# Kernel optimization log

Hardware: AMD Instinct MI355X
Metric: run time of the kernel (lower is better)

Reference implementation:

```python
import jax, jax.numpy as jnp
import numpy as np

B, S, H, T, W = 8, 512, 768, 4, 10
NEG = -1e9

def _u(key, shape, k):
    return jax.random.uniform(key, shape, jnp.float32, -k, k)

def setup_inputs():
    key = jax.random.key(0)
    ks = jax.random.split(key, 20)
    kh = float(1.0 / np.sqrt(H)); kt = float(1.0 / np.sqrt(T))
    return dict(
        embeddings=jax.random.normal(ks[0], (B, S, H), jnp.float32),
        l1f_wih=_u(ks[1], (4 * H, H), kh), l1f_whh=_u(ks[2], (4 * H, H), kh), l1f_b=_u(ks[3], (4 * H,), kh),
        l1r_wih=_u(ks[4], (4 * H, H), kh), l1r_whh=_u(ks[5], (4 * H, H), kh), l1r_b=_u(ks[6], (4 * H,), kh),
        attn_w=_u(ks[7], (3 * H,), kh), attn_b=_u(ks[8], (1,), kh),
        l2f_wih=_u(ks[9], (4 * T, 2 * H), kt), l2f_whh=_u(ks[10], (4 * T, T), kt), l2f_b=_u(ks[11], (4 * T,), kt),
        l2r_wih=_u(ks[12], (4 * T, 2 * H), kt), l2r_whh=_u(ks[13], (4 * T, T), kt), l2r_b=_u(ks[14], (4 * T,), kt),
        crf_start=0.1 * jax.random.normal(ks[15], (T,), jnp.float32),
        crf_end=0.1 * jax.random.normal(ks[16], (T,), jnp.float32),
        crf_trans=0.1 * jax.random.normal(ks[17], (T, T), jnp.float32),
        window_size=W,
    )

def _lstm_dir(x, w_ih, w_hh, b):
    # x: [B,S,D] -> [B,S,Hh]; torch gate order i,f,g,o
    Hh = w_hh.shape[1]
    bs = x.shape[0]
    xs = (jnp.einsum('bsd,gd->bsg', x, w_ih) + b).transpose(1, 0, 2)  # [S,B,4Hh]
    def step(carry, xt):
        h, c = carry
        g = xt + h @ w_hh.T
        i, f, gg, o = jnp.split(g, 4, axis=-1)
        c = jax.nn.sigmoid(f) * c + jax.nn.sigmoid(i) * jnp.tanh(gg)
        h = jax.nn.sigmoid(o) * jnp.tanh(c)
        return (h, c), h
    init = (jnp.zeros((bs, Hh), x.dtype), jnp.zeros((bs, Hh), x.dtype))
    _, hs = jax.lax.scan(step, init, xs)
    return hs.transpose(1, 0, 2)

def _bilstm(x, pf, pr):
    hf = _lstm_dir(x, *pf)
    hr = _lstm_dir(x[:, ::-1], *pr)[:, ::-1]
    return jnp.concatenate([hf, hr], axis=-1)

def _win_attn(h, w, b, win):
    # h: [B,S,D]; similarity(hi,hj) = w1.hi + w2.hj + w3.(hi*hj) + b
    bs, s, d = h.shape
    w1, w2, w3 = w[:d], w[d:2 * d], w[2 * d:]
    offs = jnp.arange(-win, win + 1)                      # [K]
    idx = jnp.arange(s)[:, None] + offs[None, :]          # [S,K]
    valid = (idx >= 0) & (idx < s)
    idxc = jnp.clip(idx, 0, s - 1)
    hw = h[:, idxc]                                       # [B,S,K,D]
    scores = (h @ w1)[:, :, None] \
        + jnp.einsum('bskd,d->bsk', hw, w2) \
        + jnp.einsum('bsd,bskd->bsk', h * w3, hw) + b[0]
    scores = jnp.where(valid[None], scores, NEG)
    aw = jax.nn.softmax(scores, axis=-1)                  # [B,S,K]
    return jnp.einsum('bsk,bskd->bsd', aw, hw)

def _viterbi(em, start, end, trans):
    # em: [B,S,T] -> tags [B,S]
    score0 = start[None] + em[:, 0]
    ems = em.transpose(1, 0, 2)[1:]                       # [S-1,B,T]
    def step(score, e_t):
        nxt = score[:, :, None] + trans[None]             # [B,Tprev,T]
        best = jnp.max(nxt, axis=1) + e_t
        bp = jnp.argmax(nxt, axis=1)
        return best, bp
    final, bps = jax.lax.scan(step, score0, ems)          # bps [S-1,B,T]
    final = final + end[None]
    last = jnp.argmax(final, axis=-1)                     # [B]
    def back(tag, bp):
        prev = jnp.take_along_axis(bp, tag[:, None], axis=1)[:, 0]
        return prev, prev
    _, tags_rev = jax.lax.scan(back, last, bps[::-1])
    return jnp.concatenate([tags_rev[::-1], last[None]], axis=0).transpose(1, 0)

def reference(embeddings, l1f_wih, l1f_whh, l1f_b, l1r_wih, l1r_whh, l1r_b,
              attn_w, attn_b, l2f_wih, l2f_whh, l2f_b, l2r_wih, l2r_whh, l2r_b,
              crf_start, crf_end, crf_trans, window_size):
    h1 = _bilstm(embeddings, (l1f_wih, l1f_whh, l1f_b), (l1r_wih, l1r_whh, l1r_b))
    d = h1.shape[-1] // 2
    hs = h1[..., :d] + h1[..., d:]                        # sum of directions [B,S,H]
    att = _win_attn(hs, attn_w, attn_b, int(window_size))
    x2 = jnp.concatenate([hs, att], axis=-1)              # [B,S,2H]
    h2 = _bilstm(x2, (l2f_wih, l2f_whh, l2f_b), (l2r_wih, l2r_whh, l2r_b))
    d2 = h2.shape[-1] // 2
    em = h2[..., :d2] + h2[..., d2:]                      # CRF emissions [B,S,T]
    tags = _viterbi(em, crf_start, crf_end, crf_trans)
    return tags, em
```

## Files before the change

### kernel.cpp

```cpp
#include <hip/hip_runtime.h>
#include <math.h>

#define SEQ 512
#define BATCH 8
#define HID 768
#define G4 3072
#define CHUNK 128
#define NEGV (-1000000000.0f)

typedef float v4f __attribute__((ext_vector_type(4)));

__device__ __forceinline__ float sigm(float x) { return 1.0f / (1.0f + expf(-x)); }

__device__ __forceinline__ float wred(float x) {
#pragma unroll
  for (int off = 32; off > 0; off >>= 1) x += __shfl_xor(x, off, 64);
  return x;
}

__device__ __forceinline__ void load2_f4_sc(const float* p0, const float* p1,
                                            v4f& a, v4f& b) {
  asm volatile("global_load_dwordx4 %0, %2, off sc0 sc1\n\t"
               "global_load_dwordx4 %1, %3, off sc0 sc1\n\t"
               "s_waitcnt vmcnt(0)"
               : "=&v"(a), "=&v"(b) : "v"(p0), "v"(p1) : "memory");
}
__device__ __forceinline__ int load_i_sc(const int* p) {
  int r;
  asm volatile("global_load_dword %0, %1, off sc0 sc1\n\ts_waitcnt vmcnt(0)"
               : "=v"(r) : "v"(p) : "memory");
  return r;
}
__device__ __forceinline__ void store_f_sc(float* p, float v) {
  asm volatile("global_store_dword %0, %1, off sc0 sc1" :: "v"(p), "v"(v) : "memory");
}
__device__ __forceinline__ void store_i_sc(int* p, int v) {
  asm volatile("global_store_dword %0, %1, off sc0 sc1" :: "v"(p), "v"(v) : "memory");
}

template <int CTRL, int RMASK>
__device__ __forceinline__ float dpp_add(float x) {
  int y = __builtin_amdgcn_update_dpp(0, __float_as_int(x), CTRL, RMASK, 0xF, false);
  return x + __int_as_float(y);
}
__device__ __forceinline__ float reduce32(float x) {
  x = dpp_add<0x121, 0xF>(x);
  x = dpp_add<0x122, 0xF>(x);
  x = dpp_add<0x124, 0xF>(x);
  x = dpp_add<0x128, 0xF>(x);
  x = dpp_add<0x142, 0xA>(x);
  return x;
}

__global__ void k_init(float* __restrict__ hbuf, int* __restrict__ flags) {
  int i = blockIdx.x * blockDim.x + threadIdx.x;
  if (i < 2 * 2 * BATCH * HID) hbuf[i] = 0.0f;
  if (i < 4096) flags[i] = 0;
}

__global__ __launch_bounds__(256) void k_proj1(
    const float* __restrict__ emb,
    const float* __restrict__ w_f, const float* __restrict__ b_f,
    const float* __restrict__ w_r, const float* __restrict__ b_r,
    float* __restrict__ xs_f, float* __restrict__ xs_r, int chunk) {
  __shared__ float As[16][132];
  __shared__ float Bs[16][132];
  const int tid = threadIdx.x;
  const int bn0 = blockIdx.x * 128;
  const int bb  = blockIdx.y;
  const int dir = blockIdx.z;
  const float* W    = dir ? w_r : w_f;
  const float* bias = dir ? b_r : b_f;
  float* xs = dir ? xs_r : xs_f;

  float acc[8][8];
#pragma unroll
  for (int i = 0; i < 8; i++)
#pragma unroll
    for (int j = 0; j < 8; j++) acc[i][j] = 0.0f;

  const int mload = tid & 127;
  const int kq0   = tid >> 7;
  const int tglob = dir ? (SEQ - 1 - (chunk * CHUNK + mload)) : (chunk * CHUNK + mload);
  const float* arow = emb + (size_t)(bb * SEQ + tglob) * HID;
  const float* brow = W + (size_t)(bn0 + mload) * HID;
  const int tm = tid & 15, tn = tid >> 4;

  for (int kt = 0; kt < HID; kt += 16) {
#pragma unroll
    for (int rep = 0; rep < 2; rep++) {
      int kq = kq0 + rep * 2;
      float4 a = *(const float4*)(arow + kt + kq * 4);
      As[kq * 4 + 0][mload] = a.x; As[kq * 4 + 1][mload] = a.y;
      As[kq * 4 + 2][mload] = a.z; As[kq * 4 + 3][mload] = a.w;
      float4 b = *(const float4*)(brow + kt + kq * 4);
      Bs[kq * 4 + 0][mload] = b.x; Bs[kq * 4 + 1][mload] = b.y;
      Bs[kq * 4 + 2][mload] = b.z; Bs[kq * 4 + 3][mload] = b.w;
    }
    __syncthreads();
#pragma unroll
    for (int k = 0; k < 16; k++) {
      float4 a0 = *(const float4*)&As[k][tm * 8];
      float4 a1 = *(const float4*)&As[k][tm * 8 + 4];
      float4 b0 = *(const float4*)&Bs[k][tn * 8];
      float4 b1 = *(const float4*)&Bs[k][tn * 8 + 4];
      float av[8] = {a0.x, a0.y, a0.z, a0.w, a1.x, a1.y, a1.z, a1.w};
      float bv[8] = {b0.x, b0.y, b0.z, b0.w, b1.x, b1.y, b1.z, b1.w};
#pragma unroll
      for (int i = 0; i < 8; i++)
#pragma unroll
        for (int j = 0; j < 8; j++) acc[i][j] += av[i] * bv[j];
    }
    __syncthreads();
  }
#pragma unroll
  for (int i = 0; i < 8; i++) {
    int row = tm * 8 + i;
    size_t base = (size_t)(bb * CHUNK + row) * G4 + bn0 + tn * 8;
#pragma unroll
    for (int j = 0; j < 8; j++) xs[base + j] = acc[i][j] + bias[bn0 + tn * 8 + j];
  }
}

__global__ __launch_bounds__(384, 2) void k_rec1(
    const float* __restrict__ whh_f, const float* __restrict__ whh_r,
    const float* __restrict__ xs_f, const float* __restrict__ xs_r,
    float* __restrict__ hbuf, float* __restrict__ cbuf, int* __restrict__ flags,
    float* __restrict__ hf, float* __restrict__ hr, int t0, int init) {
  __shared__ float hlds[4 * HID];
  __shared__ float psl[192];
  const int tid = threadIdx.x;
  const int bid = blockIdx.x;
  const int dir = bid >> 7;
  const int bh  = (bid >> 6) & 1;
  const int jb  = bid & 63;
  const int J0  = jb * 12;
  const int grp = dir * 2 + bh;
  const int g  = tid >> 5;
  const int kq = tid & 31;
  const int j  = J0 + g;
  const int ej = tid >> 2;
  const int eb = tid & 3;

  const float* W  = dir ? whh_r : whh_f;
  const float* xs = dir ? xs_r  : xs_f;
  float* harr = dir ? hr : hf;

  float wreg[4][24];
#pragma unroll
  for (int gate = 0; gate < 4; gate++) {
#pragma unroll
    for (int q = 0; q < 6; q++) {
      *(v4f*)&wreg[gate][q * 4] =
          *(const v4f*)&W[(size_t)(gate * HID + j) * HID + q * 128 + kq * 4];
    }
  }

  float cc = 0.0f;
  if (!init && tid < 48) cc = cbuf[bid * 48 + tid];

  for (int stp = 0; stp < CHUNK; stp++) {
    const int s = t0 + stp;
    const int par = s & 1;

    float exs0 = 0.f, exs1 = 0.f, exs2 = 0.f, exs3 = 0.f;
    if (tid < 48) {
      const size_t xbase = (size_t)((bh * 4 + eb) * CHUNK + stp) * G4 + J0 + ej;
      exs0 = xs[xbase + 0 * HID];
      exs1 = xs[xbase + 1 * HID];
      exs2 = xs[xbase + 2 * HID];
      exs3 = xs[xbase + 3 * HID];
    }
    if (tid < 64) {
      const int* fp = flags + (grp * 64 + tid) * 16;
      while (load_i_sc(fp) < s) { __builtin_amdgcn_s_sleep(1); }
    }
    __syncthreads();

    {
      const float* src = hbuf + (size_t)((par * 2 + dir) * BATCH + bh * 4) * HID + tid * 8;
      v4f a, b4;
      load2_f4_sc(src, src + 4, a, b4);
      *(v4f*)&hlds[tid * 8]     = a;
      *(v4f*)&hlds[tid * 8 + 4] = b4;
    }
    __syncthreads();

    float hk[4][24];
#pragma unroll
    for (int b = 0; b < 4; b++)
#pragma unroll
      for (int q = 0; q < 6; q++)
        *(v4f*)&hk[b][q * 4] = *(const v4f*)&hlds[b * HID + q * 128 + kq * 4];

    float acc[4][4];
#pragma unroll
    for (int gate = 0; gate < 4; gate++)
#pragma unroll
      for (int b = 0; b < 4; b++) acc[gate][b] = 0.0f;
#pragma unroll
    for (int b = 0; b < 4; b++)
#pragma unroll
      for (int gate = 0; gate < 4; gate++)
#pragma unroll
        for (int k = 0; k < 24; k++) acc[gate][b] += wreg[gate][k] * hk[b][k];

#pragma unroll
    for (int gate = 0; gate < 4; gate++)
#pragma unroll
      for (int b = 0; b < 4; b++) acc[gate][b] = reduce32(acc[gate][b]);

    if (kq == 16) {
#pragma unroll
      for (int gate = 0; gate < 4; gate++)
#pragma unroll
        for (int b = 0; b < 4; b++) psl[(g * 4 + gate) * 4 + b] = acc[gate][b];
    }
    __syncthreads();

    if (tid < 48) {
      float iv = psl[(ej * 4 + 0) * 4 + eb] + exs0;
      float fv = psl[(ej * 4 + 1) * 4 + eb] + exs1;
      float gv = psl[(ej * 4 + 2) * 4 + eb] + exs2;
      float ov = psl[(ej * 4 + 3) * 4 + eb] + exs3;
      cc = sigm(fv) * cc + sigm(iv) * tanhf(gv);
      float h = sigm(ov) * tanhf(cc);
      const int t = dir ? (SEQ - 1 - s) : s;
      const int bg = bh * 4 + eb;
      store_f_sc(hbuf + (size_t)(((par ^ 1) * 2 + dir) * BATCH + bg) * HID + J0 + ej, h);
      harr[(size_t)(bg * SEQ + t) * HID + J0 + ej] = h;
    }
    if (tid < 64) {
      asm volatile("s_waitcnt vmcnt(0)" ::: "memory");
      if (tid == 0) store_i_sc(flags + (grp * 64 + jb) * 16, s + 1);
    }
  }
  if (tid < 48) cbuf[bid * 48 + tid] = cc;
}

__global__ __launch_bounds__(64) void k_attn(
    const float* __restrict__ hf, const float* __restrict__ hr,
    const float* __restrict__ attn_w, const float* __restrict__ attn_b,
    float* __restrict__ att) {
  const int l = threadIdx.x;
  const int s = blockIdx.x, b = blockIdx.y;
  const size_t rbase = (size_t)(b * SEQ + s) * HID;
  float v[12];
  float u1p = 0.0f;
#pragma unroll
  for (int jj = 0; jj < 12; jj++) {
    int d = l + 64 * jj;
    float x = hf[rbase + d] + hr[rbase + d];
    u1p += x * attn_w[d];
    v[jj] = attn_w[HID + d] + x * attn_w[2 * HID + d];
  }
  float u1 = wred(u1p) + attn_b[0];
  float sc[21];
  for (int o = 0; o < 21; o++) {
    int s2 = s + o - 10;
    if (s2 >= 0 && s2 < SEQ) {
      const size_t b2 = (size_t)(b * SEQ + s2) * HID;
      float p = 0.0f;
#pragma unroll
      for (int jj = 0; jj < 12; jj++) {
        int d = l + 64 * jj;
        p += (hf[b2 + d] + hr[b2 + d]) * v[jj];
      }
      sc[o] = wred(p) + u1;
    } else {
      sc[o] = NEGV;
    }
  }
  float m = sc[0];
#pragma unroll
  for (int o = 1; o < 21; o++) m = fmaxf(m, sc[o]);
  float sum = 0.0f;
#pragma unroll
  for (int o = 0; o < 21; o++) { sc[o] = expf(sc[o] - m); sum += sc[o]; }
  float inv = 1.0f / sum;
  float acc[12];
#pragma unroll
  for (int jj = 0; jj < 12; jj++) acc[jj] = 0.0f;
  for (int o = 0; o < 21; o++) {
    int s2 = s + o - 10;
    if (s2 < 0 || s2 >= SEQ) continue;
    float a = sc[o] * inv;
    const size_t b2 = (size_t)(b * SEQ + s2) * HID;
#pragma unroll
    for (int jj = 0; jj < 12; jj++) {
      int d = l + 64 * jj;
      acc[jj] += a * (hf[b2 + d] + hr[b2 + d]);
    }
  }
  float* orow = att + rbase;
#pragma unroll
  for (int jj = 0; jj < 12; jj++) orow[l + 64 * jj] = acc[jj];
}

__global__ __launch_bounds__(256) void k_proj2(
    const float* __restrict__ hf, const float* __restrict__ hr,
    const float* __restrict__ att,
    const float* __restrict__ w2f, const float* __restrict__ b2f,
    const float* __restrict__ w2r, const float* __restrict__ b2r,
    float* __restrict__ xs2) {
  __shared__ __align__(16) float x2[2 * HID];
  __shared__ float part[32][9];
  const int tid = threadIdx.x;
  const int s = blockIdx.x, b = blockIdx.y;
  size_t base = (size_t)(b * SEQ + s) * HID;
  for (int i = tid; i < 2 * HID; i += 256)
    x2[i] = (i < HID) ? (hf[base + i] + hr[base + i]) : att[base + i - HID];
  __syncthreads();
  const int gid = tid & 31, pp = tid >> 5;
  const int d = gid >> 4, g = gid & 15;
  const float4* w4 = (const float4*)((d ? w2r : w2f) + (size_t)g * (2 * HID));
  const float4* x4 = (const float4*)x2;
  float p = 0.0f;
  for (int e = pp * 48; e < pp * 48 + 48; e++) {
    float4 xv = x4[e];
    float4 wv = w4[e];
    p += xv.x * wv.x + xv.y * wv.y + xv.z * wv.z + xv.w * wv.w;
  }
  part[gid][pp] = p;
  __syncthreads();
  if (tid < 32) {
    float sumv = (d ? b2r : b2f)[g];
#pragma unroll
    for (int q = 0; q < 8; q++) sumv += part[gid][q];
    xs2[(size_t)((d * BATCH + b) * SEQ + s) * 16 + g] = sumv;
  }
}

__global__ __launch_bounds__(1024) void k_rec2(
    const float* __restrict__ xs2,
    const float* __restrict__ whh_f, const float* __restrict__ whh_r,
    float* __restrict__ h2) {
  const int tid = threadIdx.x;
  const int w = tid >> 6;
  const int l = tid & 63;
  const int d = w >> 3, b = w & 7;
  const int hb = d * BATCH + b;
  if (l < 16) {
    const float* whh = (d ? whh_r : whh_f) + l * 4;
    const float w0 = whh[0], w1 = whh[1], w2 = whh[2], w3 = whh[3];
    const float* xrow = xs2 + (size_t)hb * SEQ * 16 + l;
    float c = 0.0f, hval = 0.0f;
    float xcur = xrow[(d ? (SEQ - 1) : 0) * 16];
    for (int st = 0; st < SEQ; st++) {
      const int t = d ? (SEQ - 1 - st) : st;
      const int tn = d ? (SEQ - 2 - st) : (st + 1);
      float xnext = (st + 1 < SEQ) ? xrow[tn * 16] : 0.0f;
      float h0 = __shfl(hval, 0, 64);
      float h1 = __shfl(hval, 1, 64);
      float h2v = __shfl(hval, 2, 64);
      float h3 = __shfl(hval, 3, 64);
      float gv = xcur + w0 * h0 + w1 * h1 + w2 * h2v + w3 * h3;
      float iv = __shfl(gv, (l & 3) + 0, 64);
      float fv = __shfl(gv, (l & 3) + 4, 64);
      float gg = __shfl(gv, (l & 3) + 8, 64);
      float ov = __shfl(gv, (l & 3) + 12, 64);
      if (l < 4) {
        c = sigm(fv) * c + sigm(iv) * tanhf(gg);
        hval = sigm(ov) * tanhf(c);
        h2[((size_t)hb * SEQ + t) * 4 + l] = hval;
      }
      xcur = xnext;
    }
  }
}

__global__ void k_em(const float* __restrict__ h2, float* __restrict__ out) {
  int i = blockIdx.x * 256 + threadIdx.x;
  if (i < BATCH * SEQ * 4) out[BATCH * SEQ + i] = h2[i] + h2[BATCH * SEQ * 4 + i];
}

__global__ __launch_bounds__(32) void k_viterbi(
    float* __restrict__ out, const float* __restrict__ start,
    const float* __restrict__ endw, const float* __restrict__ trans) {
  __shared__ unsigned char bp[SEQ - 1][32];
  const int l = threadIdx.x;
  const int b = l >> 2, j = l & 3;
  const float* em = out + BATCH * SEQ;
  const float tr0 = trans[0 * 4 + j], tr1 = trans[1 * 4 + j];
  const float tr2 = trans[2 * 4 + j], tr3 = trans[3 * 4 + j];
  float score = start[j] + em[((size_t)b * SEQ + 0) * 4 + j];
  for (int t = 1; t < SEQ; t++) {
    float s0 = __shfl(score, b * 4 + 0, 64);
    float s1 = __shfl(score, b * 4 + 1, 64);
    float s2 = __shfl(score, b * 4 + 2, 64);
    float s3 = __shfl(score, b * 4 + 3, 64);
    float v0 = s0 + tr0, v1 = s1 + tr1, v2 = s2 + tr2, v3 = s3 + tr3;
    float best = v0; int arg = 0;
    if (v1 > best) { best = v1; arg = 1; }
    if (v2 > best) { best = v2; arg = 2; }
    if (v3 > best) { best = v3; arg = 3; }
    bp[t - 1][l] = (unsigned char)arg;
    score = best + em[((size_t)b * SEQ + t) * 4 + j];
  }
  score += endw[j];
  float f0 = __shfl(score, b * 4 + 0, 64);
  float f1 = __shfl(score, b * 4 + 1, 64);
  float f2 = __shfl(score, b * 4 + 2, 64);
  float f3 = __shfl(score, b * 4 + 3, 64);
  if (j == 0) {
    float bbv = f0; int last = 0;
    if (f1 > bbv) { bbv = f1; last = 1; }
    if (f2 > bbv) { bbv = f2; last = 2; }
    if (f3 > bbv) { bbv = f3; last = 3; }
    int tag = last;
    out[b * SEQ + (SEQ - 1)] = (float)tag;
    for (int t = SEQ - 2; t >= 0; t--) {
      tag = bp[t][b * 4 + tag];
      out[b * SEQ + t] = (float)tag;
    }
  }
}

extern "C" void kernel_launch(void* const* d_in, const int* in_sizes, int n_in,
                              void* d_out, int out_size, void* d_ws, size_t ws_size,
                              hipStream_t stream) {
  const float* emb      = (const float*)d_in[0];
  const float* l1f_wih  = (const float*)d_in[1];
  const float* l1f_whh  = (const float*)d_in[2];
  const float* l1f_b    = (const float*)d_in[3];
  const float* l1r_wih  = (const float*)d_in[4];
  const float* l1r_whh  = (const float*)d_in[5];
  const float* l1r_b    = (const float*)d_in[6];
  const float* attn_w   = (const float*)d_in[7];
  const float* attn_b   = (const float*)d_in[8];
  const float* l2f_wih  = (const float*)d_in[9];
  const float* l2f_whh  = (const float*)d_in[10];
  const float* l2f_b    = (const float*)d_in[11];
  const float* l2r_wih  = (const float*)d_in[12];
  const float* l2r_whh  = (const float*)d_in[13];
  const float* l2r_b    = (const float*)d_in[14];
  const float* crf_start= (const float*)d_in[15];
  const float* crf_end  = (const float*)d_in[16];
  const float* crf_trans= (const float*)d_in[17];

  float* ws = (float*)d_ws;
  const size_t NCH = (size_t)BATCH * CHUNK * G4;
  float* xs_f = ws;
  float* xs_r = xs_f + NCH;
  float* hf   = xs_r + NCH;
  float* hr   = hf + (size_t)BATCH * SEQ * HID;
  float* hbuf = hr + (size_t)BATCH * SEQ * HID;
  float* cbuf = hbuf + 2 * 2 * BATCH * HID;
  float* h2   = cbuf + 256 * 48;
  int*   flags= (int*)(h2 + 2 * BATCH * SEQ * 4);
  float* xs2  = xs_f;
  float* att  = xs_r;

  k_init<<<dim3(96), dim3(256), 0, stream>>>(hbuf, flags);

  for (int c = 0; c < 4; c++) {
    k_proj1<<<dim3(24, 8, 2), dim3(256), 0, stream>>>(
        emb, l1f_wih, l1f_b, l1r_wih, l1r_b, xs_f, xs_r, c);
    k_rec1<<<dim3(256), dim3(384), 0, stream>>>(
        l1f_whh, l1r_whh, xs_f, xs_r, hbuf, cbuf, flags, hf, hr,
        c * CHUNK, c == 0 ? 1 : 0);
  }

  k_attn<<<dim3(SEQ, BATCH), dim3(64), 0, stream>>>(hf, hr, attn_w, attn_b, att);
  k_proj2<<<dim3(SEQ, BATCH), dim3(256), 0, stream>>>(
      hf, hr, att, l2f_wih, l2f_b, l2r_wih, l2r_b, xs2);
  k_rec2<<<dim3(1), dim3(1024), 0, stream>>>(xs2, l2f_whh, l2r_whh, h2);
  k_em<<<dim3(64), dim3(256), 0, stream>>>(h2, (float*)d_out);
  k_viterbi<<<dim3(1), dim3(32), 0, stream>>>((float*)d_out, crf_start, crf_end, crf_trans);
}
```

Before: 4.049 ms.

## Replace flag-based step barrier with per-value sequence-tagged hidden state exchange

The layer-1 recurrence no longer spins on per-block flags and then reloads the hidden state. Each hidden value is now written together with its step counter as a single 8-byte store, and readers poll the tagged data directly until every tag matches the current step. This removes the separate flag store/wait round trip and one block barrier per timestep, at the cost of doubling hbuf traffic and spinning on data loads. Separately, the direction sum hf+hr is precomputed once in a new k_sum kernel, so attention and proj2 no longer re-add it on every read.

```diff
diff --git a/kernel.cpp b/kernel.cpp
--- a/kernel.cpp
+++ b/kernel.cpp
@@ -9,6 +9,8 @@
 #define NEGV (-1000000000.0f)
 
 typedef float v4f __attribute__((ext_vector_type(4)));
+typedef int   v4i __attribute__((ext_vector_type(4)));
+typedef int   v2i __attribute__((ext_vector_type(2)));
 
 __device__ __forceinline__ float sigm(float x) { return 1.0f / (1.0f + expf(-x)); }
 
@@ -18,24 +20,18 @@
   return x;
 }
 
-__device__ __forceinline__ void load2_f4_sc(const float* p0, const float* p1,
-                                            v4f& a, v4f& b) {
-  asm volatile("global_load_dwordx4 %0, %2, off sc0 sc1\n\t"
-               "global_load_dwordx4 %1, %3, off sc0 sc1\n\t"
+__device__ __forceinline__ void load4_x4_sc(const int* p, v4i& a0, v4i& a1,
+                                            v4i& a2, v4i& a3) {
+  asm volatile("global_load_dwordx4 %0, %4, off sc0 sc1\n\t"
+               "global_load_dwordx4 %1, %4, off offset:16 sc0 sc1\n\t"
+               "global_load_dwordx4 %2, %4, off offset:32 sc0 sc1\n\t"
+               "global_load_dwordx4 %3, %4, off offset:48 sc0 sc1\n\t"
                "s_waitcnt vmcnt(0)"
-               : "=&v"(a), "=&v"(b) : "v"(p0), "v"(p1) : "memory");
-}
-__device__ __forceinline__ int load_i_sc(const int* p) {
-  int r;
-  asm volatile("global_load_dword %0, %1, off sc0 sc1\n\ts_waitcnt vmcnt(0)"
-               : "=v"(r) : "v"(p) : "memory");
-  return r;
-}
-__device__ __forceinline__ void store_f_sc(float* p, float v) {
-  asm volatile("global_store_dword %0, %1, off sc0 sc1" :: "v"(p), "v"(v) : "memory");
-}
-__device__ __forceinline__ void store_i_sc(int* p, int v) {
-  asm volatile("global_store_dword %0, %1, off sc0 sc1" :: "v"(p), "v"(v) : "memory");
+               : "=&v"(a0), "=&v"(a1), "=&v"(a2), "=&v"(a3)
+               : "v"(p) : "memory");
+}
+__device__ __forceinline__ void store_x2_sc(int* p, v2i v) {
+  asm volatile("global_store_dwordx2 %0, %1, off sc0 sc1" :: "v"(p), "v"(v) : "memory");
 }
 
 template <int CTRL, int RMASK>
@@ -52,10 +48,10 @@
   return x;
 }
 
-__global__ void k_init(float* __restrict__ hbuf, int* __restrict__ flags) {
+__global__ void k_init(int* __restrict__ hbuf) {
   int i = blockIdx.x * blockDim.x + threadIdx.x;
-  if (i < 2 * 2 * BATCH * HID) hbuf[i] = 0.0f;
-  if (i < 4096) flags[i] = 0;
+  int stride = gridDim.x * blockDim.x;
+  for (int idx = i; idx < 2 * 2 * BATCH * HID * 2; idx += stride) hbuf[idx] = 0;
 }
 
 __global__ __launch_bounds__(256) void k_proj1(
@@ -125,7 +121,7 @@
 __global__ __launch_bounds__(384, 2) void k_rec1(
     const float* __restrict__ whh_f, const float* __restrict__ whh_r,
     const float* __restrict__ xs_f, const float* __restrict__ xs_r,
-    float* __restrict__ hbuf, float* __restrict__ cbuf, int* __restrict__ flags,
+    int* __restrict__ hbuf, float* __restrict__ cbuf,
     float* __restrict__ hf, float* __restrict__ hr, int t0, int init) {
   __shared__ float hlds[4 * HID];
   __shared__ float psl[192];
@@ -135,7 +131,6 @@
   const int bh  = (bid >> 6) & 1;
   const int jb  = bid & 63;
   const int J0  = jb * 12;
-  const int grp = dir * 2 + bh;
   const int g  = tid >> 5;
   const int kq = tid & 31;
   const int j  = J0 + g;
@@ -146,6 +141,10 @@
   const float* xs = dir ? xs_r  : xs_f;
   float* harr = dir ? hr : hf;
 
+  const int le  = tid * 8;
+  const int bl  = le / HID;
+  const int jj0 = le - bl * HID;
+
   float wreg[4][24];
 #pragma unroll
   for (int gate = 0; gate < 4; gate++) {
@@ -161,7 +160,6 @@
 
   for (int stp = 0; stp < CHUNK; stp++) {
     const int s = t0 + stp;
-    const int par = s & 1;
 
     float exs0 = 0.f, exs1 = 0.f, exs2 = 0.f, exs3 = 0.f;
     if (tid < 48) {
@@ -171,18 +169,25 @@
       exs2 = xs[xbase + 2 * HID];
       exs3 = xs[xbase + 3 * HID];
     }
-    if (tid < 64) {
-      const int* fp = flags + (grp * 64 + tid) * 16;
-      while (load_i_sc(fp) < s) { __builtin_amdgcn_s_sleep(1); }
-    }
-    __syncthreads();
 
     {
-      const float* src = hbuf + (size_t)((par * 2 + dir) * BATCH + bh * 4) * HID + tid * 8;
-      v4f a, b4;
-      load2_f4_sc(src, src + 4, a, b4);
-      *(v4f*)&hlds[tid * 8]     = a;
-      *(v4f*)&hlds[tid * 8 + 4] = b4;
+      const int rslot = (s + 1) & 1;
+      const int* src = hbuf +
+          ((size_t)((rslot * 2 + dir) * BATCH + bh * 4 + bl) * HID + jj0) * 2;
+      v4i a0, a1, a2, a3;
+      for (;;) {
+        load4_x4_sc(src, a0, a1, a2, a3);
+        if ((a0.y == s) & (a0.w == s) & (a1.y == s) & (a1.w == s) &
+            (a2.y == s) & (a2.w == s) & (a3.y == s) & (a3.w == s)) break;
+        __builtin_amdgcn_s_sleep(2);
+      }
+      v4f h0, h1;
+      h0.x = __int_as_float(a0.x); h0.y = __int_as_float(a0.z);
+      h0.z = __int_as_float(a1.x); h0.w = __int_as_float(a1.z);
+      h1.x = __int_as_float(a2.x); h1.y = __int_as_float(a2.z);
+      h1.z = __int_as_float(a3.x); h1.w = __int_as_float(a3.z);
+      *(v4f*)&hlds[bl * HID + jj0]     = h0;
+      *(v4f*)&hlds[bl * HID + jj0 + 4] = h1;
     }
     __syncthreads();
 
@@ -227,30 +232,35 @@
       float h = sigm(ov) * tanhf(cc);
       const int t = dir ? (SEQ - 1 - s) : s;
       const int bg = bh * 4 + eb;
-      store_f_sc(hbuf + (size_t)(((par ^ 1) * 2 + dir) * BATCH + bg) * HID + J0 + ej, h);
+      const int wslot = s & 1;
+      v2i pv; pv.x = __float_as_int(h); pv.y = s + 1;
+      store_x2_sc(hbuf + ((size_t)((wslot * 2 + dir) * BATCH + bg) * HID + J0 + ej) * 2, pv);
       harr[(size_t)(bg * SEQ + t) * HID + J0 + ej] = h;
     }
-    if (tid < 64) {
-      asm volatile("s_waitcnt vmcnt(0)" ::: "memory");
-      if (tid == 0) store_i_sc(flags + (grp * 64 + jb) * 16, s + 1);
-    }
   }
   if (tid < 48) cbuf[bid * 48 + tid] = cc;
 }
 
+__global__ void k_sum(float* __restrict__ hf, const float* __restrict__ hr) {
+  int i = blockIdx.x * 256 + threadIdx.x;
+  float4 a = ((const float4*)hf)[i];
+  float4 b = ((const float4*)hr)[i];
+  a.x += b.x; a.y += b.y; a.z += b.z; a.w += b.w;
+  ((float4*)hf)[i] = a;
+}
+
 __global__ __launch_bounds__(64) void k_attn(
-    const float* __restrict__ hf, const float* __restrict__ hr,
-    const float* __restrict__ attn_w, const float* __restrict__ attn_b,
-    float* __restrict__ att) {
+    const float* __restrict__ hs, const float* __restrict__ attn_w,
+    const float* __restrict__ attn_b, float* __restrict__ att) {
   const int l = threadIdx.x;
   const int s = blockIdx.x, b = blockIdx.y;
-  const size_t rbase = (size_t)(b * SEQ + s) * HID;
+  const float* hrow = hs + (size_t)(b * SEQ + s) * HID;
   float v[12];
   float u1p = 0.0f;
 #pragma unroll
   for (int jj = 0; jj < 12; jj++) {
     int d = l + 64 * jj;
-    float x = hf[rbase + d] + hr[rbase + d];
+    float x = hrow[d];
     u1p += x * attn_w[d];
     v[jj] = attn_w[HID + d] + x * attn_w[2 * HID + d];
   }
@@ -259,13 +269,10 @@
   for (int o = 0; o < 21; o++) {
     int s2 = s + o - 10;
     if (s2 >= 0 && s2 < SEQ) {
-      const size_t b2 = (size_t)(b * SEQ + s2) * HID;
+      const float* h2 = hs + (size_t)(b * SEQ + s2) * HID;
       float p = 0.0f;
 #pragma unroll
-      for (int jj = 0; jj < 12; jj++) {
-        int d = l + 64 * jj;
-        p += (hf[b2 + d] + hr[b2 + d]) * v[jj];
-      }
+      for (int jj = 0; jj < 12; jj++) p += h2[l + 64 * jj] * v[jj];
       sc[o] = wred(p) + u1;
     } else {
       sc[o] = NEGV;
@@ -285,21 +292,17 @@
     int s2 = s + o - 10;
     if (s2 < 0 || s2 >= SEQ) continue;
     float a = sc[o] * inv;
-    const size_t b2 = (size_t)(b * SEQ + s2) * HID;
-#pragma unroll
-    for (int jj = 0; jj < 12; jj++) {
-      int d = l + 64 * jj;
-      acc[jj] += a * (hf[b2 + d] + hr[b2 + d]);
-    }
-  }
-  float* orow = att + rbase;
+    const float* h2 = hs + (size_t)(b * SEQ + s2) * HID;
+#pragma unroll
+    for (int jj = 0; jj < 12; jj++) acc[jj] += a * h2[l + 64 * jj];
+  }
+  float* orow = att + (size_t)(b * SEQ + s) * HID;
 #pragma unroll
   for (int jj = 0; jj < 12; jj++) orow[l + 64 * jj] = acc[jj];
 }
 
 __global__ __launch_bounds__(256) void k_proj2(
-    const float* __restrict__ hf, const float* __restrict__ hr,
-    const float* __restrict__ att,
+    const float* __restrict__ hs, const float* __restrict__ att,
     const float* __restrict__ w2f, const float* __restrict__ b2f,
     const float* __restrict__ w2r, const float* __restrict__ b2r,
     float* __restrict__ xs2) {
@@ -309,7 +312,7 @@
   const int s = blockIdx.x, b = blockIdx.y;
   size_t base = (size_t)(b * SEQ + s) * HID;
   for (int i = tid; i < 2 * HID; i += 256)
-    x2[i] = (i < HID) ? (hf[base + i] + hr[base + i]) : att[base + i - HID];
+    x2[i] = (i < HID) ? hs[base + i] : att[base + i - HID];
   __syncthreads();
   const int gid = tid & 31, pp = tid >> 5;
   const int d = gid >> 4, g = gid & 15;
@@ -440,30 +443,32 @@
 
   float* ws = (float*)d_ws;
   const size_t NCH = (size_t)BATCH * CHUNK * G4;
+  const size_t BSH = (size_t)BATCH * SEQ * HID;
   float* xs_f = ws;
   float* xs_r = xs_f + NCH;
   float* hf   = xs_r + NCH;
-  float* hr   = hf + (size_t)BATCH * SEQ * HID;
-  float* hbuf = hr + (size_t)BATCH * SEQ * HID;
-  float* cbuf = hbuf + 2 * 2 * BATCH * HID;
-  float* h2   = cbuf + 256 * 48;
-  int*   flags= (int*)(h2 + 2 * BATCH * SEQ * 4);
+  float* hr   = hf + BSH;
+  float* h2   = hr + BSH;
+  float* cbuf = h2 + 2 * BATCH * SEQ * 4;
+  int*   hbuf = (int*)(cbuf + 256 * 48);
   float* xs2  = xs_f;
   float* att  = xs_r;
-
-  k_init<<<dim3(96), dim3(256), 0, stream>>>(hbuf, flags);
+  float* hs   = hf;
+
+  k_init<<<dim3(96), dim3(256), 0, stream>>>(hbuf);
 
   for (int c = 0; c < 4; c++) {
     k_proj1<<<dim3(24, 8, 2), dim3(256), 0, stream>>>(
         emb, l1f_wih, l1f_b, l1r_wih, l1r_b, xs_f, xs_r, c);
     k_rec1<<<dim3(256), dim3(384), 0, stream>>>(
-        l1f_whh, l1r_whh, xs_f, xs_r, hbuf, cbuf, flags, hf, hr,
+        l1f_whh, l1r_whh, xs_f, xs_r, hbuf, cbuf, hf, hr,
         c * CHUNK, c == 0 ? 1 : 0);
   }
 
-  k_attn<<<dim3(SEQ, BATCH), dim3(64), 0, stream>>>(hf, hr, attn_w, attn_b, att);
+  k_sum<<<dim3(3072), dim3(256), 0, stream>>>(hf, hr);
+  k_attn<<<dim3(SEQ, BATCH), dim3(64), 0, stream>>>(hs, attn_w, attn_b, att);
   k_proj2<<<dim3(SEQ, BATCH), dim3(256), 0, stream>>>(
-      hf, hr, att, l2f_wih, l2f_b, l2r_wih, l2r_b, xs2);
+      hs, att, l2f_wih, l2f_b, l2r_wih, l2r_b, xs2);
   k_rec2<<<dim3(1), dim3(1024), 0, stream>>>(xs2, l2f_whh, l2r_whh, h2);
   k_em<<<dim3(64), dim3(256), 0, stream>>>(h2, (float*)d_out);
   k_viterbi<<<dim3(1), dim3(32), 0, stream>>>((float*)d_out, crf_start, crf_end, crf_trans);
```

New measurement: 6.087 ms. 1.5x slower.
